# Kernel tuning notes

Measured on AMD Instinct MI355X. Metric: run time of the kernel, lower is better.

Reference implementation:

```python
import jax, jax.numpy as jnp
import numpy as np

B, P, D_MODEL = 16, 256, 1024
V, D_LLM = 1000, 4096
H, DK = 16, 64  # d_keys = d_model // n_heads


def setup_inputs() -> dict:
    key = jax.random.key(0)
    ks = jax.random.split(key, 11)
    s = lambda k, shape, fan: jax.random.normal(k, shape, jnp.float32) / np.sqrt(fan)
    return {
        "target_embedding": jax.random.normal(ks[0], (B, P, D_MODEL), jnp.float32),
        "source_embedding": jax.random.normal(ks[1], (V, D_LLM), jnp.float32),
        "value_embedding": jax.random.normal(ks[2], (V, D_LLM), jnp.float32),
        "Wq": s(ks[3], (D_MODEL, H * DK), D_MODEL),
        "bq": jnp.zeros((H * DK,), jnp.float32),
        "Wk": s(ks[4], (D_LLM, H * DK), D_LLM),
        "bk": jnp.zeros((H * DK,), jnp.float32),
        "Wv": s(ks[5], (D_LLM, H * DK), D_LLM),
        "bv": jnp.zeros((H * DK,), jnp.float32),
        "Wo": s(ks[6], (H * DK, D_LLM), H * DK),
        "bo": jnp.zeros((D_LLM,), jnp.float32),
    }


def reference(target_embedding, source_embedding, value_embedding,
              Wq, bq, Wk, bk, Wv, bv, Wo, bo):
    b, p, _ = target_embedding.shape
    v = source_embedding.shape[0]
    # projections
    Q = (target_embedding @ Wq + bq).reshape(b, p, H, DK)   # bphd
    K = (source_embedding @ Wk + bk).reshape(v, H, DK)      # vhd
    Vv = (value_embedding @ Wv + bv).reshape(v, H, DK)      # vhd
    scale = 1.0 / np.sqrt(DK)
    # NOTE: non-standard einsum — contracts over v, elementwise in d
    scores = jnp.einsum('bphd,vhd->bhpd', Q, K)             # [B,H,P,DK]
    A = jax.nn.softmax(scale * scores, axis=-1)             # softmax over head dim d
    # (dropout is identity in eval mode)
    R = jnp.einsum('bhpd,vhd->bphd', A, Vv)                 # A * sum_v V
    out = R.reshape(b, p, H * DK) @ Wo + bo                 # [B,P,D_LLM]
    return out
```

## Files before the change

### kernel.cpp

```cpp
#include <hip/hip_runtime.h>

#define BB   16
#define PP   256
#define BP   4096
#define DMODEL 1024
#define VV   1000
#define DLLM 4096
#define HH   16
#define DK   64
#define HDK  1024

using f32x4 = __attribute__((ext_vector_type(4))) float;
using s16x8 = __attribute__((ext_vector_type(8))) short;

__device__ __forceinline__ unsigned short f2bf(float f) {
    unsigned int u = __builtin_bit_cast(unsigned int, f);
    u = (u + 0x7FFFu + ((u >> 16) & 1u)) >> 16;
    return (unsigned short)u;
}

__device__ __forceinline__ void gload_lds16(const unsigned short* g, unsigned short* lds) {
    __builtin_amdgcn_global_load_lds(
        (const __attribute__((address_space(1))) void*)g,
        (__attribute__((address_space(3))) void*)lds,
        16, 0, 0);
}

__device__ __forceinline__ void transpose_body(const float* __restrict__ src,
                                               unsigned short* __restrict__ dst,
                                               int R, int C, int bx, int by, int t,
                                               float (*tile)[33]) {
    int tx = t & 31, ty = t >> 5;
    int c0 = bx * 32, r0 = by * 32;
#pragma unroll
    for (int j = 0; j < 4; ++j)
        tile[ty + j * 8][tx] = src[(size_t)(r0 + ty + j * 8) * C + c0 + tx];
    __syncthreads();
#pragma unroll
    for (int j = 0; j < 4; ++j)
        dst[(size_t)(c0 + ty + j * 8) * R + r0 + tx] = f2bf(tile[tx][ty + j * 8]);
}

__global__ void mega1(const float* __restrict__ src0, const float* __restrict__ src1,
                      float* __restrict__ part1,
                      const float* __restrict__ target, unsigned short* __restrict__ tgt_bf,
                      const float* __restrict__ Wq, unsigned short* __restrict__ wq_t,
                      const float* __restrict__ Wo, unsigned short* __restrict__ wo_t) {
    __shared__ float tile[32][33];
    int b = blockIdx.x, t = threadIdx.x;
    if (b < 1280) {
        int x = b & 15, y = (b >> 4) % 40, z = b / 640;
        int col = x * 256 + t;
        const float* src = z ? src1 : src0;
        int r0 = y * 25;
        float acc = 0.f;
        for (int r = 0; r < 25; ++r)
            acc += src[(size_t)(r0 + r) * DLLM + col];
        part1[((z * 40 + y) * DLLM) + col] = acc;
    } else if (b < 1280 + 4096) {
        int idx = (b - 1280) * 256 + t;
        float4 v = reinterpret_cast<const float4*>(target)[idx];
        ushort4 o = make_ushort4(f2bf(v.x), f2bf(v.y), f2bf(v.z), f2bf(v.w));
        reinterpret_cast<ushort4*>(tgt_bf)[idx] = o;
    } else if (b < 1280 + 4096 + 1024) {
        int b2 = b - 5376;
        transpose_body(Wq, wq_t, DMODEL, HDK, b2 & 31, b2 >> 5, t, tile);
    } else {
        int b2 = b - 6400;
        transpose_body(Wo, wo_t, HDK, DLLM, b2 & 127, b2 >> 7, t, tile);
    }
}

__global__ void gemv_partial2(const float* __restrict__ Wk, const float* __restrict__ Wv,
                              const float* __restrict__ part1, float* __restrict__ part2) {
    __shared__ float vec[64];
    int c     = blockIdx.x * 256 + threadIdx.x;
    int chunk = blockIdx.y;
    int z     = blockIdx.z;
    const float* W = z ? Wv : Wk;
    if (threadIdx.x < 64) {
        int r = chunk * 64 + threadIdx.x;
        float a = 0.f;
        for (int p = 0; p < 40; ++p)
            a += part1[(size_t)(z * 40 + p) * DLLM + r];
        vec[threadIdx.x] = a;
    }
    __syncthreads();
    float acc = 0.f;
    int r0 = chunk * 64;
    for (int r = 0; r < 64; ++r)
        acc += vec[r] * W[(size_t)(r0 + r) * HDK + c];
    part2[((z * 64 + chunk) * HDK) + c] = acc;
}

__global__ void gemv_reduce(const float* __restrict__ part,
                            const float* __restrict__ bk, const float* __restrict__ bv,
                            float* __restrict__ kvsum) {
    int idx = blockIdx.x * 256 + threadIdx.x;
    int z = idx >> 10, c = idx & 1023;
    float acc = 0.f;
    for (int ch = 0; ch < 64; ++ch) acc += part[(size_t)(z * 64 + ch) * HDK + c];
    acc += (float)VV * (z ? bv[c] : bk[c]);
    kvsum[idx] = acc;
}

template<int EPI, int BMt, int BNt, int WM, int WN>
__global__ __launch_bounds__(WM * WN * 64, 2)
void gemm_ctd(const unsigned short* __restrict__ A, const unsigned short* __restrict__ Bt,
              float* __restrict__ C, const float* __restrict__ bias,
              const float* __restrict__ kvsum, unsigned short* __restrict__ R,
              int N, int K, int gx) {
    constexpr int WAVES = WM * WN;
    constexpr int M_REP = BMt / WM / 16;
    __shared__ unsigned short Asm[4][BMt * 32];
    __shared__ unsigned short Bsm[4][BNt * 32];

    const int nwg = gridDim.x, q = nwg >> 3;
    const int nb = (blockIdx.x & 7) * q + (blockIdx.x >> 3);
    const int bm = (nb / gx) * BMt;
    const int bn = (nb % gx) * BNt;

    const int t = threadIdx.x;
    const int w = t >> 6, lane = t & 63;
    const int wr = w / WN, wc = w % WN;
    const int l15 = lane & 15, kgrp = lane >> 4;

    size_t goffA[2], goffB[2];
    int ldso[2];
    {
        int s8 = lane & 7, jj = lane >> 3;
#pragma unroll
        for (int i = 0; i < 2; ++i) {
            int sr = (i * WAVES + w) * 8 + jj;
            int x = s8 ^ (sr & 7);
            int row = sr * 2 + (x >> 2);
            int col = (x & 3) * 8;
            goffA[i] = (size_t)(bm + row) * K + col;
            goffB[i] = (size_t)(bn + row) * K + col;
            ldso[i] = (i * WAVES + w) * 512;
        }
    }
    int ra[M_REP], rb[4];
#pragma unroll
    for (int m = 0; m < M_REP; ++m) {
        int r = wr * (M_REP * 16) + m * 16 + l15;
        int s8 = (kgrp + 4 * (r & 1)) ^ ((r >> 1) & 7);
        ra[m] = (r >> 1) * 64 + s8 * 8;
    }
#pragma unroll
    for (int n = 0; n < 4; ++n) {
        int r = wc * 64 + n * 16 + l15;
        int s8 = (kgrp + 4 * (r & 1)) ^ ((r >> 1) & 7);
        rb[n] = (r >> 1) * 64 + s8 * 8;
    }

    f32x4 acc[M_REP][4] = {};

#define STAGE(t_, b_) do { size_t k0_ = (size_t)(t_) * 32;            \
    gload_lds16(A + goffA[0] + k0_, &Asm[b_][ldso[0]]);               \
    gload_lds16(A + goffA[1] + k0_, &Asm[b_][ldso[1]]);               \
    gload_lds16(Bt + goffB[0] + k0_, &Bsm[b_][ldso[0]]);              \
    gload_lds16(Bt + goffB[1] + k0_, &Bsm[b_][ldso[1]]); } while (0)

    const int nT = K >> 5;
    STAGE(0, 0); STAGE(1, 1); STAGE(2, 2);
    asm volatile("s_waitcnt vmcnt(8)" ::: "memory");
    __builtin_amdgcn_s_barrier();

    for (int tk = 0; tk < nT; ++tk) {
        const int b = tk & 3;
        s16x8 af[M_REP], bfr[4];
#pragma unroll
        for (int m = 0; m < M_REP; ++m)
            af[m] = *reinterpret_cast<const s16x8*>(&Asm[b][ra[m]]);
#pragma unroll
        for (int n = 0; n < 4; ++n)
            bfr[n] = *reinterpret_cast<const s16x8*>(&Bsm[b][rb[n]]);
        if (tk < nT - 3) STAGE(tk + 3, (tk + 3) & 3);
        __builtin_amdgcn_s_setprio(1);
#pragma unroll
        for (int m = 0; m < M_REP; ++m)
#pragma unroll
            for (int n = 0; n < 4; ++n)
                acc[m][n] = __builtin_amdgcn_mfma_f32_16x16x32_bf16(af[m], bfr[n], acc[m][n], 0, 0, 0);
        __builtin_amdgcn_s_setprio(0);
        if (tk < nT - 3)       asm volatile("s_waitcnt vmcnt(8)" ::: "memory");
        else if (tk == nT - 3) asm volatile("s_waitcnt vmcnt(4)" ::: "memory");
        else if (tk == nT - 2) asm volatile("s_waitcnt vmcnt(0)" ::: "memory");
        if (tk + 1 < nT) __builtin_amdgcn_s_barrier();
    }
#undef STAGE

    if (EPI == 0) {
#pragma unroll
        for (int m = 0; m < M_REP; ++m) {
            int grow = bm + wr * (M_REP * 16) + m * 16 + kgrp * 4;
#pragma unroll
            for (int n = 0; n < 4; ++n) {
                int gcol = bn + wc * 64 + n * 16 + l15;
                float bb = bias[gcol];
#pragma unroll
                for (int j = 0; j < 4; ++j)
                    C[(size_t)(grow + j) * N + gcol] = acc[m][n][j] + bb;
            }
        }
    } else {
        float bqv[4], ksv[4], vsv[4];
#pragma unroll
        for (int n = 0; n < 4; ++n) {
            int col = bn + wc * 64 + n * 16 + l15;
            bqv[n] = bias[col];
            ksv[n] = kvsum[col];
            vsv[n] = kvsum[HDK + col];
        }
#pragma unroll
        for (int m = 0; m < M_REP; ++m) {
            int grow = bm + wr * (M_REP * 16) + m * 16 + kgrp * 4;
#pragma unroll
            for (int j = 0; j < 4; ++j) {
                float x[4];
#pragma unroll
                for (int n = 0; n < 4; ++n)
                    x[n] = 0.125f * (acc[m][n][j] + bqv[n]) * ksv[n];
                float mx = fmaxf(fmaxf(x[0], x[1]), fmaxf(x[2], x[3]));
#pragma unroll
                for (int off = 8; off; off >>= 1) mx = fmaxf(mx, __shfl_xor(mx, off));
                float e[4], s = 0.f;
#pragma unroll
                for (int n = 0; n < 4; ++n) { e[n] = __expf(x[n] - mx); s += e[n]; }
#pragma unroll
                for (int off = 8; off; off >>= 1) s += __shfl_xor(s, off);
                float inv = 1.0f / s;
#pragma unroll
                for (int n = 0; n < 4; ++n) {
                    int col = bn + wc * 64 + n * 16 + l15;
                    R[(size_t)(grow + j) * N + col] = f2bf(e[n] * inv * vsv[n]);
                }
            }
        }
    }
}

extern "C" void kernel_launch(void* const* d_in, const int* in_sizes, int n_in,
                              void* d_out, int out_size, void* d_ws, size_t ws_size,
                              hipStream_t stream) {
    const float* target = (const float*)d_in[0];
    const float* source = (const float*)d_in[1];
    const float* value  = (const float*)d_in[2];
    const float* Wq = (const float*)d_in[3];
    const float* bq = (const float*)d_in[4];
    const float* Wk = (const float*)d_in[5];
    const float* bk = (const float*)d_in[6];
    const float* Wv = (const float*)d_in[7];
    const float* bv = (const float*)d_in[8];
    const float* Wo = (const float*)d_in[9];
    const float* bo = (const float*)d_in[10];
    float* out = (float*)d_out;

    char* ws = (char*)d_ws;
    float*          part1  = (float*)(ws);
    float*          part2  = (float*)(ws + 0x180000);
    float*          kvsum  = (float*)(ws + 0x210000);
    unsigned short* tgt_bf = (unsigned short*)(ws + 0x400000);
    unsigned short* wq_t   = (unsigned short*)(ws + 0xC00000);
    unsigned short* wo_t   = (unsigned short*)(ws + 0xE00000);
    unsigned short* Rb     = (unsigned short*)(ws + 0x1600000);

    mega1<<<10496, 256, 0, stream>>>(source, value, part1, target, tgt_bf, Wq, wq_t, Wo, wo_t);

    gemv_partial2<<<dim3(4, 64, 2), 256, 0, stream>>>(Wk, Wv, part1, part2);
    gemv_reduce<<<8, 256, 0, stream>>>(part2, bk, bv, kvsum);

    gemm_ctd<1, 128, 128, 2, 2><<<256, 256, 0, stream>>>(
        tgt_bf, wq_t, nullptr, bq, kvsum, Rb, HDK, DMODEL, HDK / 128);

    gemm_ctd<0, 256, 256, 2, 4><<<256, 512, 0, stream>>>(
        Rb, wo_t, out, bo, nullptr, nullptr, DLLM, HDK, DLLM / 256);
}
```

Baseline: 95.27 us.

## Restructure GEMM main loop into four-phase ping-pong schedule with K=64 tiles

Replaces the 4-buffer K=32 pipeline in both bf16 GEMMs with a double-buffered K=64 tile and splits each iteration into four MFMA quadrants. Partial A/B loads for later tiles are interleaved between the quadrants, with barriers and priority changes between them. The aim is to overlap global-to-LDS traffic and LDS reads with matrix core work more finely and to halve the number of loop iterations. It adds many more barriers per iteration, relies on carefully counted vmcnt waits, and uses a new swizzle layout.

```diff
diff --git a/kernel.cpp b/kernel.cpp
--- a/kernel.cpp
+++ b/kernel.cpp
@@ -106,17 +106,21 @@
 
 template<int EPI, int BMt, int BNt, int WM, int WN>
 __global__ __launch_bounds__(WM * WN * 64, 2)
-void gemm_ctd(const unsigned short* __restrict__ A, const unsigned short* __restrict__ Bt,
-              float* __restrict__ C, const float* __restrict__ bias,
-              const float* __restrict__ kvsum, unsigned short* __restrict__ R,
-              int N, int K, int gx) {
+void gemm_p4(const unsigned short* __restrict__ A, const unsigned short* __restrict__ Bt,
+             float* __restrict__ C, const float* __restrict__ bias,
+             const float* __restrict__ kvsum, unsigned short* __restrict__ R,
+             int N, int K, int gx) {
     constexpr int WAVES = WM * WN;
-    constexpr int M_REP = BMt / WM / 16;
-    __shared__ unsigned short Asm[4][BMt * 32];
-    __shared__ unsigned short Bsm[4][BNt * 32];
-
-    const int nwg = gridDim.x, q = nwg >> 3;
-    const int nb = (blockIdx.x & 7) * q + (blockIdx.x >> 3);
+    constexpr int Mw = BMt / WM;
+    constexpr int M_REP = Mw / 16;
+    constexpr int M2 = M_REP / 2;
+    static_assert(BNt / WN == 64, "wave col span must be 64");
+
+    __shared__ __align__(16) unsigned short Asm[2][BMt * 64];
+    __shared__ __align__(16) unsigned short Bsm[2][BNt * 64];
+
+    const int nwg = gridDim.x, q8 = nwg >> 3;
+    const int nb = (blockIdx.x & 7) * q8 + (blockIdx.x >> 3);
     const int bm = (nb / gx) * BMt;
     const int bn = (nb % gx) * BNt;
 
@@ -125,76 +129,121 @@
     const int wr = w / WN, wc = w % WN;
     const int l15 = lane & 15, kgrp = lane >> 4;
 
-    size_t goffA[2], goffB[2];
-    int ldso[2];
-    {
-        int s8 = lane & 7, jj = lane >> 3;
+    const int scol = ((lane & 7) ^ (lane >> 3)) * 8;
+    const int srow = lane >> 3;
+
+    const int so0 = ((kgrp ^ (lane & 7)) * 8);
+    const int so1 = so0 ^ 32;
+    const int rbA = (wr * Mw + l15) * 64;
+    const int rbB = (wc * 64 + l15) * 64;
+
+    f32x4 acc[M_REP][4] = {};
+
+    auto stageA = [&](int qq, int tt, int bb) {
 #pragma unroll
         for (int i = 0; i < 2; ++i) {
-            int sr = (i * WAVES + w) * 8 + jj;
-            int x = s8 ^ (sr & 7);
-            int row = sr * 2 + (x >> 2);
-            int col = (x & 3) * 8;
-            goffA[i] = (size_t)(bm + row) * K + col;
-            goffB[i] = (size_t)(bn + row) * K + col;
-            ldso[i] = (i * WAVES + w) * 512;
-        }
+            int rb = i * (BMt / 2) + qq * (BMt / 4) + w * 8;
+            gload_lds16(A + (size_t)(bm + rb + srow) * K + tt * 64 + scol,
+                        &Asm[bb][rb * 64]);
+        }
+    };
+    auto stageB = [&](int hh, int tt, int bb) {
+#pragma unroll
+        for (int i = 0; i < 2; ++i) {
+            int p = i * (BNt / 128) + (w >> 2);
+            int rb = p * 64 + hh * 32 + (w & 3) * 8;
+            gload_lds16(Bt + (size_t)(bn + rb + srow) * K + tt * 64 + scol,
+                        &Bsm[bb][rb * 64]);
+        }
+    };
+
+    const int nT = K >> 6;
+    stageA(0, 0, 0); stageA(1, 0, 0); stageB(0, 0, 0); stageB(1, 0, 0);
+    asm volatile("s_waitcnt vmcnt(4)" ::: "memory");
+    stageA(0, 1, 1); stageA(1, 1, 1); stageB(0, 1, 1);
+    asm volatile("s_waitcnt vmcnt(6)" ::: "memory");
+    __builtin_amdgcn_s_barrier();
+
+    for (int tk = 0; tk < nT; ++tk) {
+        const int b = tk & 1, ob = b ^ 1;
+        s16x8 af0[M2][2], af1[M2][2], bf0[2][2], bf1[2][2];
+#pragma unroll
+        for (int m = 0; m < M2; ++m) {
+            af0[m][0] = *reinterpret_cast<const s16x8*>(&Asm[b][rbA + m * 1024 + so0]);
+            af0[m][1] = *reinterpret_cast<const s16x8*>(&Asm[b][rbA + m * 1024 + so1]);
+        }
+#pragma unroll
+        for (int n = 0; n < 2; ++n) {
+            bf0[n][0] = *reinterpret_cast<const s16x8*>(&Bsm[b][rbB + n * 1024 + so0]);
+            bf0[n][1] = *reinterpret_cast<const s16x8*>(&Bsm[b][rbB + n * 1024 + so1]);
+        }
+        if (tk + 1 < nT) stageB(1, tk + 1, ob);
+        __builtin_amdgcn_s_barrier();
+        __builtin_amdgcn_s_setprio(1);
+#pragma unroll
+        for (int m = 0; m < M2; ++m)
+#pragma unroll
+            for (int n = 0; n < 2; ++n)
+#pragma unroll
+                for (int kk = 0; kk < 2; ++kk)
+                    acc[m][n] = __builtin_amdgcn_mfma_f32_16x16x32_bf16(af0[m][kk], bf0[n][kk], acc[m][n], 0, 0, 0);
+        __builtin_amdgcn_s_setprio(0);
+        __builtin_amdgcn_s_barrier();
+#pragma unroll
+        for (int m = 0; m < M2; ++m) {
+            af1[m][0] = *reinterpret_cast<const s16x8*>(&Asm[b][rbA + (M2 + m) * 1024 + so0]);
+            af1[m][1] = *reinterpret_cast<const s16x8*>(&Asm[b][rbA + (M2 + m) * 1024 + so1]);
+        }
+        if (tk + 2 < nT) stageA(0, tk + 2, b);
+        if (tk == nT - 1) asm volatile("s_waitcnt vmcnt(0)" ::: "memory");
+        __builtin_amdgcn_s_barrier();
+        __builtin_amdgcn_s_setprio(1);
+#pragma unroll
+        for (int m = 0; m < M2; ++m)
+#pragma unroll
+            for (int n = 0; n < 2; ++n)
+#pragma unroll
+                for (int kk = 0; kk < 2; ++kk)
+                    acc[M2 + m][n] = __builtin_amdgcn_mfma_f32_16x16x32_bf16(af1[m][kk], bf0[n][kk], acc[M2 + m][n], 0, 0, 0);
+        __builtin_amdgcn_s_setprio(0);
+        __builtin_amdgcn_s_barrier();
+#pragma unroll
+        for (int n = 0; n < 2; ++n) {
+            bf1[n][0] = *reinterpret_cast<const s16x8*>(&Bsm[b][rbB + (2 + n) * 1024 + so0]);
+            bf1[n][1] = *reinterpret_cast<const s16x8*>(&Bsm[b][rbB + (2 + n) * 1024 + so1]);
+        }
+        if (tk + 2 < nT) stageA(1, tk + 2, b);
+        __builtin_amdgcn_s_barrier();
+        __builtin_amdgcn_s_setprio(1);
+#pragma unroll
+        for (int m = 0; m < M2; ++m)
+#pragma unroll
+            for (int n = 0; n < 2; ++n)
+#pragma unroll
+                for (int kk = 0; kk < 2; ++kk)
+                    acc[M2 + m][2 + n] = __builtin_amdgcn_mfma_f32_16x16x32_bf16(af1[m][kk], bf1[n][kk], acc[M2 + m][2 + n], 0, 0, 0);
+        __builtin_amdgcn_s_setprio(0);
+        __builtin_amdgcn_s_barrier();
+        if (tk + 2 < nT) stageB(0, tk + 2, b);
+        if (tk + 2 < nT)      asm volatile("s_waitcnt vmcnt(6)" ::: "memory");
+        else if (tk + 1 < nT) asm volatile("s_waitcnt vmcnt(2)" ::: "memory");
+        __builtin_amdgcn_s_barrier();
+        __builtin_amdgcn_s_setprio(1);
+#pragma unroll
+        for (int m = 0; m < M2; ++m)
+#pragma unroll
+            for (int n = 0; n < 2; ++n)
+#pragma unroll
+                for (int kk = 0; kk < 2; ++kk)
+                    acc[m][2 + n] = __builtin_amdgcn_mfma_f32_16x16x32_bf16(af0[m][kk], bf1[n][kk], acc[m][2 + n], 0, 0, 0);
+        __builtin_amdgcn_s_setprio(0);
+        __builtin_amdgcn_s_barrier();
     }
-    int ra[M_REP], rb[4];
-#pragma unroll
-    for (int m = 0; m < M_REP; ++m) {
-        int r = wr * (M_REP * 16) + m * 16 + l15;
-        int s8 = (kgrp + 4 * (r & 1)) ^ ((r >> 1) & 7);
-        ra[m] = (r >> 1) * 64 + s8 * 8;
-    }
-#pragma unroll
-    for (int n = 0; n < 4; ++n) {
-        int r = wc * 64 + n * 16 + l15;
-        int s8 = (kgrp + 4 * (r & 1)) ^ ((r >> 1) & 7);
-        rb[n] = (r >> 1) * 64 + s8 * 8;
-    }
-
-    f32x4 acc[M_REP][4] = {};
-
-#define STAGE(t_, b_) do { size_t k0_ = (size_t)(t_) * 32;            \
-    gload_lds16(A + goffA[0] + k0_, &Asm[b_][ldso[0]]);               \
-    gload_lds16(A + goffA[1] + k0_, &Asm[b_][ldso[1]]);               \
-    gload_lds16(Bt + goffB[0] + k0_, &Bsm[b_][ldso[0]]);              \
-    gload_lds16(Bt + goffB[1] + k0_, &Bsm[b_][ldso[1]]); } while (0)
-
-    const int nT = K >> 5;
-    STAGE(0, 0); STAGE(1, 1); STAGE(2, 2);
-    asm volatile("s_waitcnt vmcnt(8)" ::: "memory");
-    __builtin_amdgcn_s_barrier();
-
-    for (int tk = 0; tk < nT; ++tk) {
-        const int b = tk & 3;
-        s16x8 af[M_REP], bfr[4];
-#pragma unroll
-        for (int m = 0; m < M_REP; ++m)
-            af[m] = *reinterpret_cast<const s16x8*>(&Asm[b][ra[m]]);
-#pragma unroll
-        for (int n = 0; n < 4; ++n)
-            bfr[n] = *reinterpret_cast<const s16x8*>(&Bsm[b][rb[n]]);
-        if (tk < nT - 3) STAGE(tk + 3, (tk + 3) & 3);
-        __builtin_amdgcn_s_setprio(1);
-#pragma unroll
-        for (int m = 0; m < M_REP; ++m)
-#pragma unroll
-            for (int n = 0; n < 4; ++n)
-                acc[m][n] = __builtin_amdgcn_mfma_f32_16x16x32_bf16(af[m], bfr[n], acc[m][n], 0, 0, 0);
-        __builtin_amdgcn_s_setprio(0);
-        if (tk < nT - 3)       asm volatile("s_waitcnt vmcnt(8)" ::: "memory");
-        else if (tk == nT - 3) asm volatile("s_waitcnt vmcnt(4)" ::: "memory");
-        else if (tk == nT - 2) asm volatile("s_waitcnt vmcnt(0)" ::: "memory");
-        if (tk + 1 < nT) __builtin_amdgcn_s_barrier();
-    }
-#undef STAGE
 
     if (EPI == 0) {
 #pragma unroll
         for (int m = 0; m < M_REP; ++m) {
-            int grow = bm + wr * (M_REP * 16) + m * 16 + kgrp * 4;
+            int grow = bm + wr * Mw + m * 16 + kgrp * 4;
 #pragma unroll
             for (int n = 0; n < 4; ++n) {
                 int gcol = bn + wc * 64 + n * 16 + l15;
@@ -215,7 +264,7 @@
         }
 #pragma unroll
         for (int m = 0; m < M_REP; ++m) {
-            int grow = bm + wr * (M_REP * 16) + m * 16 + kgrp * 4;
+            int grow = bm + wr * Mw + m * 16 + kgrp * 4;
 #pragma unroll
             for (int j = 0; j < 4; ++j) {
                 float x[4];
@@ -271,9 +320,9 @@
     gemv_partial2<<<dim3(4, 64, 2), 256, 0, stream>>>(Wk, Wv, part1, part2);
     gemv_reduce<<<8, 256, 0, stream>>>(part2, bk, bv, kvsum);
 
-    gemm_ctd<1, 128, 128, 2, 2><<<256, 256, 0, stream>>>(
+    gemm_p4<1, 128, 128, 2, 2><<<256, 256, 0, stream>>>(
         tgt_bf, wq_t, nullptr, bq, kvsum, Rb, HDK, DMODEL, HDK / 128);
 
-    gemm_ctd<0, 256, 256, 2, 4><<<256, 512, 0, stream>>>(
+    gemm_p4<0, 256, 256, 2, 4><<<256, 512, 0, stream>>>(
         Rb, wo_t, out, bo, nullptr, nullptr, DLLM, HDK, DLLM / 256);
 }
```

Result: no change. 95.29 us (+0.0%).

## Use 3-stage LDS pipeline and smaller GEMM tiles with twice the blocks

Applied to the files above, without the earlier changes.

Reduces the GEMM LDS ring from four buffers to three and prefetches two tiles ahead, with staging counts generalised per tile shape. Both GEMM launches switch to smaller tiles (128x64 for the Q/softmax GEMM, 256x128 for the output GEMM) with 512 workgroups each. The aim is less LDS per block and more blocks in flight to fill the CUs. In exchange there is less prefetch depth and less operand reuse per tile.

```diff
diff --git a/kernel.cpp b/kernel.cpp
--- a/kernel.cpp
+++ b/kernel.cpp
@@ -106,17 +106,24 @@
 
 template<int EPI, int BMt, int BNt, int WM, int WN>
 __global__ __launch_bounds__(WM * WN * 64, 2)
-void gemm_ctd(const unsigned short* __restrict__ A, const unsigned short* __restrict__ Bt,
-              float* __restrict__ C, const float* __restrict__ bias,
-              const float* __restrict__ kvsum, unsigned short* __restrict__ R,
-              int N, int K, int gx) {
+void gemm_ctd3(const unsigned short* __restrict__ A, const unsigned short* __restrict__ Bt,
+               float* __restrict__ C, const float* __restrict__ bias,
+               const float* __restrict__ kvsum, unsigned short* __restrict__ R,
+               int N, int K, int gx) {
     constexpr int WAVES = WM * WN;
-    constexpr int M_REP = BMt / WM / 16;
-    __shared__ unsigned short Asm[4][BMt * 32];
-    __shared__ unsigned short Bsm[4][BNt * 32];
-
-    const int nwg = gridDim.x, q = nwg >> 3;
-    const int nb = (blockIdx.x & 7) * q + (blockIdx.x >> 3);
+    constexpr int Mw = BMt / WM;
+    constexpr int M_REP = Mw / 16;
+    constexpr int NA = BMt * 32 / (WAVES * 512);
+    constexpr int NB = BNt * 32 / (WAVES * 512);
+    constexpr int NST = NA + NB;
+    static_assert(BNt / WN == 64, "wave col span must be 64");
+    static_assert(NA >= 1 && NB >= 1, "staging geometry");
+
+    __shared__ __align__(16) unsigned short Asm[3][BMt * 32];
+    __shared__ __align__(16) unsigned short Bsm[3][BNt * 32];
+
+    const int nwg = gridDim.x, q8 = nwg >> 3;
+    const int nb = (blockIdx.x & 7) * q8 + (blockIdx.x >> 3);
     const int bm = (nb / gx) * BMt;
     const int bn = (nb % gx) * BNt;
 
@@ -125,25 +132,29 @@
     const int wr = w / WN, wc = w % WN;
     const int l15 = lane & 15, kgrp = lane >> 4;
 
-    size_t goffA[2], goffB[2];
-    int ldso[2];
+    size_t goffA[NA], goffB[NB];
+    int ldsoA[NA], ldsoB[NB];
     {
         int s8 = lane & 7, jj = lane >> 3;
 #pragma unroll
-        for (int i = 0; i < 2; ++i) {
+        for (int i = 0; i < NA; ++i) {
             int sr = (i * WAVES + w) * 8 + jj;
             int x = s8 ^ (sr & 7);
-            int row = sr * 2 + (x >> 2);
-            int col = (x & 3) * 8;
-            goffA[i] = (size_t)(bm + row) * K + col;
-            goffB[i] = (size_t)(bn + row) * K + col;
-            ldso[i] = (i * WAVES + w) * 512;
+            goffA[i] = (size_t)(bm + sr * 2 + (x >> 2)) * K + (x & 3) * 8;
+            ldsoA[i] = (i * WAVES + w) * 512;
+        }
+#pragma unroll
+        for (int i = 0; i < NB; ++i) {
+            int sr = (i * WAVES + w) * 8 + jj;
+            int x = s8 ^ (sr & 7);
+            goffB[i] = (size_t)(bn + sr * 2 + (x >> 2)) * K + (x & 3) * 8;
+            ldsoB[i] = (i * WAVES + w) * 512;
         }
     }
     int ra[M_REP], rb[4];
 #pragma unroll
     for (int m = 0; m < M_REP; ++m) {
-        int r = wr * (M_REP * 16) + m * 16 + l15;
+        int r = wr * Mw + m * 16 + l15;
         int s8 = (kgrp + 4 * (r & 1)) ^ ((r >> 1) & 7);
         ra[m] = (r >> 1) * 64 + s8 * 8;
     }
@@ -156,27 +167,31 @@
 
     f32x4 acc[M_REP][4] = {};
 
-#define STAGE(t_, b_) do { size_t k0_ = (size_t)(t_) * 32;            \
-    gload_lds16(A + goffA[0] + k0_, &Asm[b_][ldso[0]]);               \
-    gload_lds16(A + goffA[1] + k0_, &Asm[b_][ldso[1]]);               \
-    gload_lds16(Bt + goffB[0] + k0_, &Bsm[b_][ldso[0]]);              \
-    gload_lds16(Bt + goffB[1] + k0_, &Bsm[b_][ldso[1]]); } while (0)
+#define STAGE(t_, b_) do { size_t k0_ = (size_t)(t_) * 32;             \
+    _Pragma("unroll")                                                  \
+    for (int i_ = 0; i_ < NA; ++i_)                                    \
+        gload_lds16(A + goffA[i_] + k0_, &Asm[b_][ldsoA[i_]]);         \
+    _Pragma("unroll")                                                  \
+    for (int i_ = 0; i_ < NB; ++i_)                                    \
+        gload_lds16(Bt + goffB[i_] + k0_, &Bsm[b_][ldsoB[i_]]); } while (0)
+
+#define WAIT_VM(n_) asm volatile("s_waitcnt vmcnt(" #n_ ")" ::: "memory")
 
     const int nT = K >> 5;
-    STAGE(0, 0); STAGE(1, 1); STAGE(2, 2);
-    asm volatile("s_waitcnt vmcnt(8)" ::: "memory");
+    STAGE(0, 0); STAGE(1, 1);
+    if constexpr (NST == 6) WAIT_VM(6); else if constexpr (NST == 4) WAIT_VM(4); else WAIT_VM(3);
     __builtin_amdgcn_s_barrier();
 
+    int cur = 0;
     for (int tk = 0; tk < nT; ++tk) {
-        const int b = tk & 3;
         s16x8 af[M_REP], bfr[4];
 #pragma unroll
         for (int m = 0; m < M_REP; ++m)
-            af[m] = *reinterpret_cast<const s16x8*>(&Asm[b][ra[m]]);
+            af[m] = *reinterpret_cast<const s16x8*>(&Asm[cur][ra[m]]);
 #pragma unroll
         for (int n = 0; n < 4; ++n)
-            bfr[n] = *reinterpret_cast<const s16x8*>(&Bsm[b][rb[n]]);
-        if (tk < nT - 3) STAGE(tk + 3, (tk + 3) & 3);
+            bfr[n] = *reinterpret_cast<const s16x8*>(&Bsm[cur][rb[n]]);
+        if (tk + 2 < nT) STAGE(tk + 2, cur == 0 ? 2 : cur - 1);
         __builtin_amdgcn_s_setprio(1);
 #pragma unroll
         for (int m = 0; m < M_REP; ++m)
@@ -184,17 +199,21 @@
             for (int n = 0; n < 4; ++n)
                 acc[m][n] = __builtin_amdgcn_mfma_f32_16x16x32_bf16(af[m], bfr[n], acc[m][n], 0, 0, 0);
         __builtin_amdgcn_s_setprio(0);
-        if (tk < nT - 3)       asm volatile("s_waitcnt vmcnt(8)" ::: "memory");
-        else if (tk == nT - 3) asm volatile("s_waitcnt vmcnt(4)" ::: "memory");
-        else if (tk == nT - 2) asm volatile("s_waitcnt vmcnt(0)" ::: "memory");
+        if (tk + 2 < nT) {
+            if constexpr (NST == 6) WAIT_VM(6); else if constexpr (NST == 4) WAIT_VM(4); else WAIT_VM(3);
+        } else if (tk + 1 < nT) {
+            WAIT_VM(0);
+        }
         if (tk + 1 < nT) __builtin_amdgcn_s_barrier();
+        cur = (cur == 2) ? 0 : cur + 1;
     }
 #undef STAGE
+#undef WAIT_VM
 
     if (EPI == 0) {
 #pragma unroll
         for (int m = 0; m < M_REP; ++m) {
-            int grow = bm + wr * (M_REP * 16) + m * 16 + kgrp * 4;
+            int grow = bm + wr * Mw + m * 16 + kgrp * 4;
 #pragma unroll
             for (int n = 0; n < 4; ++n) {
                 int gcol = bn + wc * 64 + n * 16 + l15;
@@ -215,7 +234,7 @@
         }
 #pragma unroll
         for (int m = 0; m < M_REP; ++m) {
-            int grow = bm + wr * (M_REP * 16) + m * 16 + kgrp * 4;
+            int grow = bm + wr * Mw + m * 16 + kgrp * 4;
 #pragma unroll
             for (int j = 0; j < 4; ++j) {
                 float x[4];
@@ -271,9 +290,9 @@
     gemv_partial2<<<dim3(4, 64, 2), 256, 0, stream>>>(Wk, Wv, part1, part2);
     gemv_reduce<<<8, 256, 0, stream>>>(part2, bk, bv, kvsum);
 
-    gemm_ctd<1, 128, 128, 2, 2><<<256, 256, 0, stream>>>(
-        tgt_bf, wq_t, nullptr, bq, kvsum, Rb, HDK, DMODEL, HDK / 128);
-
-    gemm_ctd<0, 256, 256, 2, 4><<<256, 512, 0, stream>>>(
-        Rb, wo_t, out, bo, nullptr, nullptr, DLLM, HDK, DLLM / 256);
-}
+    gemm_ctd3<1, 128, 64, 4, 1><<<512, 256, 0, stream>>>(
+        tgt_bf, wq_t, nullptr, bq, kvsum, Rb, HDK, DMODEL, HDK / 64);
+
+    gemm_ctd3<0, 256, 128, 2, 2><<<512, 256, 0, stream>>>(
+        Rb, wo_t, out, bo, nullptr, nullptr, DLLM, HDK, DLLM / 128);
+}
```

After: 92.54 us. -2.9%, faster.
